# Kernel optimization log

Hardware: AMD Instinct MI355X
Metric: run time of the kernel (lower is better)

## Reference

```python
import jax, jax.numpy as jnp
import numpy as np

IN_NC = 7


def setup_inputs() -> dict:
    key = jax.random.key(0)
    ks = jax.random.split(key, 32)
    B, H, W = 4, 192, 192
    Cf, O, L = 64, 64, 32  # in_fea, out_fea, len=max(64//16,32)
    d = {}
    d['fea'] = jax.random.normal(ks[0], (B, Cf, H, W), jnp.float32)
    d['inputs'] = jax.random.normal(ks[1], (B, IN_NC, H, W), jnp.float32)
    j = 2
    for i in range(3):
        k = 2 * i + 1
        oc = IN_NC * 3 * k * k
        d['dw_w%d' % i] = jax.random.normal(ks[j], (Cf, 1, k, k), jnp.float32) * 0.05; j += 1
        d['dw_b%d' % i] = jnp.zeros((Cf,), jnp.float32)
        d['pw_w%d' % i] = jax.random.normal(ks[j], (oc, Cf), jnp.float32) * 0.05; j += 1
        d['pw_b%d' % i] = jnp.zeros((oc,), jnp.float32)
        d['dcn_w%d' % i] = jax.random.normal(ks[j], (O, IN_NC, k, k), jnp.float32) * 0.05; j += 1
        d['dcn_b%d' % i] = jnp.zeros((O,), jnp.float32)
    d['attn_w'] = jax.random.normal(ks[j], (O, 3 * O), jnp.float32) * 0.05; j += 1
    d['attn_b'] = jnp.zeros((O,), jnp.float32)
    d['fc_w'] = jax.random.normal(ks[j], (L, O), jnp.float32) * 0.05; j += 1
    d['fc_b'] = jnp.zeros((L,), jnp.float32)
    for i in range(3):
        d['fcs_w%d' % i] = jax.random.normal(ks[j], (O, L), jnp.float32) * 0.05; j += 1
        d['fcs_b%d' % i] = jnp.zeros((O,), jnp.float32)
    d['conv_w'] = jax.random.normal(ks[j], (O, 3 * O), jnp.float32) * 0.05; j += 1
    d['conv_b'] = jnp.zeros((O,), jnp.float32)
    return d


def _dw_conv(x, w, b):
    # depthwise conv, stride 1, SAME padding (pad = k//2 for odd k)
    y = jax.lax.conv_general_dilated(x, w, window_strides=(1, 1), padding='SAME',
                                     dimension_numbers=('NCHW', 'OIHW', 'NCHW'),
                                     feature_group_count=x.shape[1])
    return y + b[None, :, None, None]


def _pw_conv(x, w, b):
    return jnp.einsum('bchw,oc->bohw', x, w) + b[None, :, None, None]


def _mdcn(x, offset, mask, w, b, k):
    # Modulated deformable conv, deformable_groups == C (one channel per group),
    # stride 1, padding k//2. offset: [B, C*2*K, H, W] as (c, k, (dy,dx)); mask: [B, C*K, H, W].
    B, C, H, W = x.shape
    K = k * k
    pad = k // 2
    off = offset.reshape(B, C, K, 2, H, W)
    m = mask.reshape(B, C, K, H, W)
    ky = (jnp.arange(K) // k).astype(jnp.float32)
    kx = (jnp.arange(K) % k).astype(jnp.float32)
    py = off[:, :, :, 0] + (ky[:, None, None] + jnp.arange(H, dtype=jnp.float32)[None, :, None] - pad)
    px = off[:, :, :, 1] + (kx[:, None, None] + jnp.arange(W, dtype=jnp.float32)[None, None, :] - pad)
    y0 = jnp.floor(py)
    x0 = jnp.floor(px)
    wy = py - y0
    wx = px - x0
    bi = jnp.arange(B)[:, None, None, None, None]
    ci = jnp.arange(C)[None, :, None, None, None]

    def gather(yi, xi):
        valid = (yi >= 0) & (yi < H) & (xi >= 0) & (xi < W)
        yc = jnp.clip(yi, 0, H - 1).astype(jnp.int32)
        xc = jnp.clip(xi, 0, W - 1).astype(jnp.int32)
        return jnp.where(valid, x[bi, ci, yc, xc], 0.0)

    v00 = gather(y0, x0)
    v01 = gather(y0, x0 + 1)
    v10 = gather(y0 + 1, x0)
    v11 = gather(y0 + 1, x0 + 1)
    samp = (v00 * (1 - wy) * (1 - wx) + v01 * (1 - wy) * wx
            + v10 * wy * (1 - wx) + v11 * wy * wx) * m  # [B,C,K,H,W]
    O = w.shape[0]
    return jnp.einsum('bckhw,ock->bohw', samp, w.reshape(O, C, K)) + b[None, :, None, None]


def reference(fea, inputs,
              dw_w0, dw_b0, pw_w0, pw_b0, dcn_w0, dcn_b0,
              dw_w1, dw_b1, pw_w1, pw_b1, dcn_w1, dcn_b1,
              dw_w2, dw_b2, pw_w2, pw_b2, dcn_w2, dcn_b2,
              attn_w, attn_b, fc_w, fc_b,
              fcs_w0, fcs_b0, fcs_w1, fcs_b1, fcs_w2, fcs_b2,
              conv_w, conv_b):
    dw_w = [dw_w0, dw_w1, dw_w2]; dw_b = [dw_b0, dw_b1, dw_b2]
    pw_w = [pw_w0, pw_w1, pw_w2]; pw_b = [pw_b0, pw_b1, pw_b2]
    dcn_w = [dcn_w0, dcn_w1, dcn_w2]; dcn_b = [dcn_b0, dcn_b1, dcn_b2]
    fcs_w = [fcs_w0, fcs_w1, fcs_w2]; fcs_b = [fcs_b0, fcs_b1, fcs_b2]
    outs = []
    for i in range(3):
        k = 2 * i + 1
        ds = k * k
        om = _pw_conv(_dw_conv(fea, dw_w[i], dw_b[i]), pw_w[i], pw_b[i])
        offset = om[:, :IN_NC * 2 * ds]
        mask = jax.nn.sigmoid(om[:, IN_NC * 2 * ds:])
        outs.append(jax.nn.relu(_mdcn(inputs, offset, mask, dcn_w[i], dcn_b[i], k)))
    out = jnp.stack(outs, axis=1)  # [B, 3, O, H, W]
    B, T, C, H, W = out.shape
    att = jax.nn.relu(_pw_conv(out.reshape(B, T * C, H, W), attn_w, attn_b))
    att = jnp.mean(att, axis=(2, 3), keepdims=True)  # GAP -> [B, O, 1, 1]
    att = jax.nn.relu(_pw_conv(att, fc_w, fc_b))      # [B, L, 1, 1]
    atts = jnp.stack([_pw_conv(att, fcs_w[i], fcs_b[i]) for i in range(3)], axis=1)  # [B,3,O,1,1]
    out = out * atts
    out = jax.nn.relu(_pw_conv(out.reshape(B, T * C, H, W), conv_w, conv_b))
    return out
```

## Files before the change

### kernel.cpp

```cpp
#include <hip/hip_runtime.h>
#include <math.h>

#define HH 192
#define WW 192
#define HWP (192*192)
#define BB 4
#define CF 64
#define NC 7
#define OO 64
#define NTOT (BB*HWP)
#define PIX_BLOCKS (HWP/256)
#define PBLK2 (HWP/128)

typedef float f32x16 __attribute__((ext_vector_type(16)));
typedef float f32x4  __attribute__((ext_vector_type(4)));

template<int k>
__global__ __launch_bounds__(256)
void dwv_kernel(const float* __restrict__ fea, const float* __restrict__ w,
                const float* __restrict__ bias, float* __restrict__ out) {
    constexpr int pad = k / 2;
    int idx = blockIdx.x * 256 + threadIdx.x;
    int xq = idx % 48;
    int x0 = xq * 4;
    int hpos = (idx / 48) % HH;
    int plane = idx / (48 * HH);
    int c = plane % CF;
    const float* f = fea + (size_t)plane * HWP;

    float wk[k * k];
#pragma unroll
    for (int i = 0; i < k * k; ++i) wk[i] = w[c * k * k + i];

    float acc0 = 0.f, acc1 = 0.f, acc2 = 0.f, acc3 = 0.f;
#pragma unroll
    for (int dy = 0; dy < k; ++dy) {
        int y = hpos + dy - pad;
        if (y < 0 || y >= HH) continue;
        const float* row = f + y * WW;
        float4 q0 = (x0 >= 4) ? *(const float4*)(row + x0 - 4) : make_float4(0.f, 0.f, 0.f, 0.f);
        float4 q1 = *(const float4*)(row + x0);
        float4 q2 = (x0 + 4 < WW) ? *(const float4*)(row + x0 + 4) : make_float4(0.f, 0.f, 0.f, 0.f);
        float wnd[8] = {q0.z, q0.w, q1.x, q1.y, q1.z, q1.w, q2.x, q2.y};
#pragma unroll
        for (int dx = 0; dx < k; ++dx) {
            float wt = wk[dy * k + dx];
            acc0 += wnd[0 + dx + 2 - pad] * wt;
            acc1 += wnd[1 + dx + 2 - pad] * wt;
            acc2 += wnd[2 + dx + 2 - pad] * wt;
            acc3 += wnd[3 + dx + 2 - pad] * wt;
        }
    }
    float b = bias[c];
    float4 o = make_float4(acc0 + b, acc1 + b, acc2 + b, acc3 + b);
    *(float4*)(out + (size_t)plane * HWP + hpos * WW + x0) = o;
}

__global__ void transpose_kernel(const float* __restrict__ in, float* __restrict__ out,
                                 int rows, int cols) {
    int idx = blockIdx.x * 256 + threadIdx.x;
    if (idx >= rows * cols) return;
    int r = idx / cols, c = idx % cols;
    out[c * rows + r] = in[idx];
}

__global__ void k1_fold_kernel(const float* __restrict__ pw_w, const float* __restrict__ pw_b,
                               const float* __restrict__ dw_w0, const float* __restrict__ dw_b0,
                               float* __restrict__ pw_wf, float* __restrict__ pw_bf) {
    int i = blockIdx.x * 256 + threadIdx.x;
    if (i < 21 * 64) pw_wf[i] = pw_w[i] * dw_w0[i & 63];
    if (i < 21) {
        float s = pw_b[i];
        for (int c = 0; c < 64; ++c) s += pw_w[i * 64 + c] * dw_b0[c];
        pw_bf[i] = s;
    }
}

__global__ __launch_bounds__(256)
void pw_gemm_kernel(const float* __restrict__ pw_w, const float* __restrict__ pw_b,
                    const float* __restrict__ dw, float* __restrict__ om,
                    int src0, int n_yx, int src1, int M) {
    __shared__ float As[64][68];
    __shared__ float Bs[64][132];
    const int ntiles = NTOT / 128;
    int ntile = blockIdx.x % ntiles;
    int mtile = blockIdx.x / ntiles;
    int nb0 = ntile * 128;
    int mb0 = mtile * 64;
    int tid = threadIdx.x;

    {
        int m = tid & 63;
        int kq = tid >> 6;
        int gm = mb0 + m;
        int srow = (gm < M) ? ((gm < n_yx) ? (src0 + gm) : (src1 + (gm - n_yx))) : src0;
        const float* ap = pw_w + (size_t)srow * CF;
#pragma unroll
        for (int i = 0; i < 4; ++i) {
            int k0 = (kq * 4 + i) * 4;
            float4 v = *(const float4*)(ap + k0);
            As[k0 + 0][m] = v.x; As[k0 + 1][m] = v.y;
            As[k0 + 2][m] = v.z; As[k0 + 3][m] = v.w;
        }
    }
    {
        int b = nb0 / HWP;
        int p0 = nb0 % HWP;
        const float* bp = dw + (size_t)b * CF * HWP + p0;
#pragma unroll
        for (int i = 0; i < 8; ++i) {
            int idx = tid + i * 256;
            int kk = idx >> 5;
            int f4 = idx & 31;
            float4 v = *(const float4*)(bp + (size_t)kk * HWP + f4 * 4);
            *(float4*)&Bs[kk][f4 * 4] = v;
        }
    }
    __syncthreads();

    int tm = (tid & 15) * 4;
    int tn = (tid >> 4) * 8;
    f32x4 aA0 = 0.f, aA1 = 0.f, aB0 = 0.f, aB1 = 0.f;
    f32x4 aC0 = 0.f, aC1 = 0.f, aD0 = 0.f, aD1 = 0.f;
#pragma unroll 8
    for (int kk = 0; kk < 64; ++kk) {
        f32x4 a  = *(const f32x4*)&As[kk][tm];
        f32x4 b0 = *(const f32x4*)&Bs[kk][tn];
        f32x4 b1 = *(const f32x4*)&Bs[kk][tn + 4];
#pragma unroll
        for (int j = 0; j < 4; ++j) {
            aA0[j] += a[0] * b0[j];  aA1[j] += a[0] * b1[j];
            aB0[j] += a[1] * b0[j];  aB1[j] += a[1] * b1[j];
            aC0[j] += a[2] * b0[j];  aC1[j] += a[2] * b1[j];
            aD0[j] += a[3] * b0[j];  aD1[j] += a[3] * b1[j];
        }
    }
    {
        int gm = mb0 + tm;
        float* dst = om + (size_t)gm * NTOT + nb0 + tn;
        if (gm < M) {
            float bi = pw_b[(gm < n_yx) ? (src0 + gm) : (src1 + gm - n_yx)];
#pragma unroll
            for (int j = 0; j < 4; ++j) { dst[j] = aA0[j] + bi; dst[4 + j] = aA1[j] + bi; }
        }
        gm++; dst += NTOT;
        if (gm < M) {
            float bi = pw_b[(gm < n_yx) ? (src0 + gm) : (src1 + gm - n_yx)];
#pragma unroll
            for (int j = 0; j < 4; ++j) { dst[j] = aB0[j] + bi; dst[4 + j] = aB1[j] + bi; }
        }
        gm++; dst += NTOT;
        if (gm < M) {
            float bi = pw_b[(gm < n_yx) ? (src0 + gm) : (src1 + gm - n_yx)];
#pragma unroll
            for (int j = 0; j < 4; ++j) { dst[j] = aC0[j] + bi; dst[4 + j] = aC1[j] + bi; }
        }
        gm++; dst += NTOT;
        if (gm < M) {
            float bi = pw_b[(gm < n_yx) ? (src0 + gm) : (src1 + gm - n_yx)];
#pragma unroll
            for (int j = 0; j < 4; ++j) { dst[j] = aD0[j] + bi; dst[4 + j] = aD1[j] + bi; }
        }
    }
}

template<int k>
__global__ __launch_bounds__(256)
void sample_kernel(const float* __restrict__ om, const float* __restrict__ inputs,
                   float* __restrict__ sbuf, int t0, int t1) {
    constexpr int K = k * k;
    constexpr int pad = k / 2;
    const int T = t1 - t0;
    int g = blockIdx.x / (NTOT / 256);
    int nb = blockIdx.x % (NTOT / 256);
    int n = nb * 256 + threadIdx.x;
    int b = n / HWP, p = n % HWP;
    int h = p / WW, wq = p % WW;
    const float* inb = inputs + (size_t)b * NC * HWP;
    int half = (T + 1) >> 1;
    int i0 = g * half;
    int i1 = min(T, i0 + half);
#pragma unroll 2
    for (int i = i0; i < i1; ++i) {
        int r = t0 + i;
        float oy = om[(size_t)(2 * i) * NTOT + n];
        float ox = om[(size_t)(2 * i + 1) * NTOT + n];
        float mr = om[(size_t)(2 * T + i) * NTOT + n];
        int c = r / K;
        int kk = r - c * K;
        int ky = kk / k, kx = kk - ky * k;
        const float* inc_ = inb + (size_t)c * HWP;
        float m = 1.f / (1.f + __expf(-mr));
        float py = oy + (float)(ky + h - pad);
        float px = ox + (float)(kx + wq - pad);
        float y0 = floorf(py), x0 = floorf(px);
        float wyf = py - y0, wxf = px - x0;
        int iy0 = (int)y0, ix0 = (int)x0;
        bool y0v = (iy0 >= 0) && (iy0 < HH);
        bool y1v = (iy0 + 1 >= 0) && (iy0 + 1 < HH);
        bool x0v = (ix0 >= 0) && (ix0 < WW);
        bool x1v = (ix0 + 1 >= 0) && (ix0 + 1 < WW);
        int yc0 = min(max(iy0, 0), HH - 1), yc1 = min(max(iy0 + 1, 0), HH - 1);
        int xc0 = min(max(ix0, 0), WW - 1), xc1 = min(max(ix0 + 1, 0), WW - 1);
        float v00 = 0.f, v01 = 0.f, v10 = 0.f, v11 = 0.f;
        if (y0v) {
            if (x0v) v00 = inc_[yc0 * WW + xc0];
            if (x1v) v01 = inc_[yc0 * WW + xc1];
        }
        if (y1v) {
            if (x0v) v10 = inc_[yc1 * WW + xc0];
            if (x1v) v11 = inc_[yc1 * WW + xc1];
        }
        float s = (v00 * (1.f - wyf) * (1.f - wxf) + v01 * (1.f - wyf) * wxf +
                   v10 * wyf * (1.f - wxf) + v11 * wyf * wxf) * m;
        sbuf[(size_t)i * NTOT + n] = s;
    }
}

__global__ __launch_bounds__(256)
void acc_gemm_kernel(const float* __restrict__ wt,
                     const float* __restrict__ bias,
                     const float* __restrict__ sbuf,
                     float* __restrict__ outbuf, int t_slot,
                     int t0, int t1, int flags) {
    __shared__ float As[64][68];
    __shared__ float Bs[64][132];
    const int T = t1 - t0;
    int nb0 = blockIdx.x * 128;
    int tid = threadIdx.x;

    for (int i4 = tid; i4 < T * 16; i4 += 256) {
        int row = i4 >> 4, c4 = (i4 & 15) * 4;
        float4 v = *(const float4*)(wt + (size_t)(t0 + row) * OO + c4);
        As[row][c4] = v.x; As[row][c4 + 1] = v.y; As[row][c4 + 2] = v.z; As[row][c4 + 3] = v.w;
    }
    for (int i4 = tid; i4 < T * 32; i4 += 256) {
        int row = i4 >> 5, f4 = (i4 & 31) * 4;
        float4 v = *(const float4*)(sbuf + (size_t)row * NTOT + nb0 + f4);
        *(float4*)&Bs[row][f4] = v;
    }
    __syncthreads();

    int tm = (tid & 15) * 4;
    int tn = (tid >> 4) * 8;
    f32x4 aA0 = 0.f, aA1 = 0.f, aB0 = 0.f, aB1 = 0.f;
    f32x4 aC0 = 0.f, aC1 = 0.f, aD0 = 0.f, aD1 = 0.f;
#pragma unroll 2
    for (int kk = 0; kk < T; ++kk) {
        f32x4 a  = *(const f32x4*)&As[kk][tm];
        f32x4 b0 = *(const f32x4*)&Bs[kk][tn];
        f32x4 b1 = *(const f32x4*)&Bs[kk][tn + 4];
#pragma unroll
        for (int j = 0; j < 4; ++j) {
            aA0[j] += a[0] * b0[j];  aA1[j] += a[0] * b1[j];
            aB0[j] += a[1] * b0[j];  aB1[j] += a[1] * b1[j];
            aC0[j] += a[2] * b0[j];  aC1[j] += a[2] * b1[j];
            aD0[j] += a[3] * b0[j];  aD1[j] += a[3] * b1[j];
        }
    }

    int b = nb0 / HWP, p0 = nb0 % HWP;
    f32x4 accs[8] = {aA0, aA1, aB0, aB1, aC0, aC1, aD0, aD1};
#pragma unroll
    for (int row = 0; row < 4; ++row) {
        int ch = tm + row;
        float* ptr = outbuf + ((size_t)((b * 3 + t_slot) * OO + ch)) * HWP + p0 + tn;
        f32x4 lo = accs[row * 2], hi = accs[row * 2 + 1];
        if (!(flags & 1)) {
            f32x4 o0 = *(const f32x4*)ptr;
            f32x4 o1 = *(const f32x4*)(ptr + 4);
#pragma unroll
            for (int j = 0; j < 4; ++j) { lo[j] += o0[j]; hi[j] += o1[j]; }
        }
        if (flags & 2) {
            float bi = bias[ch];
#pragma unroll
            for (int j = 0; j < 4; ++j) {
                lo[j] += bi; hi[j] += bi;
                lo[j] = lo[j] > 0.f ? lo[j] : 0.f;
                hi[j] = hi[j] > 0.f ? hi[j] : 0.f;
            }
        }
        *(f32x4*)ptr = lo;
        *(f32x4*)(ptr + 4) = hi;
    }
}

__global__ __launch_bounds__(256)
void branch_k1_kernel(const float* __restrict__ fea,
                      const float* __restrict__ dw_w0, const float* __restrict__ dw_b0,
                      const float* __restrict__ pw_w, const float* __restrict__ pw_b,
                      const float* __restrict__ inputs,
                      const float* __restrict__ dcn_wt, const float* __restrict__ dcn_b,
                      float* __restrict__ outbuf) {
    __shared__ float lw[21 * 64];
    for (int i = threadIdx.x; i < 21 * 16; i += 256)
        ((float4*)lw)[i] = ((const float4*)pw_w)[i];
    __syncthreads();
    int gid = blockIdx.x;
    int b = gid / PIX_BLOCKS;
    int p = (gid % PIX_BLOCKS) * 256 + threadIdx.x;
    int h = p / WW, wq = p % WW;
    const float* inb = inputs + (size_t)b * NC * HWP;

    f32x16 dwv0, dwv1, dwv2, dwv3;
    {
        const float* fp = fea + (size_t)(b * CF) * HWP + p;
#pragma unroll
        for (int j = 0; j < 16; ++j) dwv0[j] = fp[(size_t)j * HWP] * dw_w0[j] + dw_b0[j];
#pragma unroll
        for (int j = 0; j < 16; ++j) dwv1[j] = fp[(size_t)(16 + j) * HWP] * dw_w0[16 + j] + dw_b0[16 + j];
#pragma unroll
        for (int j = 0; j < 16; ++j) dwv2[j] = fp[(size_t)(32 + j) * HWP] * dw_w0[32 + j] + dw_b0[32 + j];
#pragma unroll
        for (int j = 0; j < 16; ++j) dwv3[j] = fp[(size_t)(48 + j) * HWP] * dw_w0[48 + j] + dw_b0[48 + j];
    }
    f32x16 acc0, acc1, acc2, acc3;
#pragma unroll
    for (int j = 0; j < 16; ++j) { acc0[j] = 0.f; acc1[j] = 0.f; acc2[j] = 0.f; acc3[j] = 0.f; }

    for (int r = 0; r < NC; ++r) {
        const float* wy = lw + (2 * r) * 64;
        const float* wx = wy + 64;
        const float* wm = lw + (14 + r) * 64;
        const float* inc_ = inb + (size_t)r * HWP;
        float oy = pw_b[2 * r], ox = pw_b[2 * r + 1], om = pw_b[14 + r];
#pragma unroll
        for (int j = 0; j < 16; ++j) { oy += wy[j] * dwv0[j];      ox += wx[j] * dwv0[j];      om += wm[j] * dwv0[j]; }
#pragma unroll
        for (int j = 0; j < 16; ++j) { oy += wy[16 + j] * dwv1[j]; ox += wx[16 + j] * dwv1[j]; om += wm[16 + j] * dwv1[j]; }
#pragma unroll
        for (int j = 0; j < 16; ++j) { oy += wy[32 + j] * dwv2[j]; ox += wx[32 + j] * dwv2[j]; om += wm[32 + j] * dwv2[j]; }
#pragma unroll
        for (int j = 0; j < 16; ++j) { oy += wy[48 + j] * dwv3[j]; ox += wx[48 + j] * dwv3[j]; om += wm[48 + j] * dwv3[j]; }
        float m = 1.f / (1.f + __expf(-om));
        float py = oy + (float)h;
        float px = ox + (float)wq;
        float y0 = floorf(py), x0 = floorf(px);
        float wyf = py - y0, wxf = px - x0;
        int iy0 = (int)y0, ix0 = (int)x0;
        bool y0v = (iy0 >= 0) && (iy0 < HH);
        bool y1v = (iy0 + 1 >= 0) && (iy0 + 1 < HH);
        bool x0v = (ix0 >= 0) && (ix0 < WW);
        bool x1v = (ix0 + 1 >= 0) && (ix0 + 1 < WW);
        int yc0 = min(max(iy0, 0), HH - 1), yc1 = min(max(iy0 + 1, 0), HH - 1);
        int xc0 = min(max(ix0, 0), WW - 1), xc1 = min(max(ix0 + 1, 0), WW - 1);
        float v00 = 0.f, v01 = 0.f, v10 = 0.f, v11 = 0.f;
        if (y0v) {
            if (x0v) v00 = inc_[yc0 * WW + xc0];
            if (x1v) v01 = inc_[yc0 * WW + xc1];
        }
        if (y1v) {
            if (x0v) v10 = inc_[yc1 * WW + xc0];
            if (x1v) v11 = inc_[yc1 * WW + xc1];
        }
        float s = (v00 * (1.f - wyf) * (1.f - wxf) + v01 * (1.f - wyf) * wxf +
                   v10 * wyf * (1.f - wxf) + v11 * wyf * wxf) * m;
        const float* dt = dcn_wt + (size_t)r * OO;
#pragma unroll
        for (int j = 0; j < 16; ++j) acc0[j] += s * dt[j];
#pragma unroll
        for (int j = 0; j < 16; ++j) acc1[j] += s * dt[16 + j];
#pragma unroll
        for (int j = 0; j < 16; ++j) acc2[j] += s * dt[32 + j];
#pragma unroll
        for (int j = 0; j < 16; ++j) acc3[j] += s * dt[48 + j];
    }
    float* op = outbuf + (size_t)(b * 3 * OO) * HWP + p;
#pragma unroll
    for (int j = 0; j < 16; ++j) { float v = acc0[j] + dcn_b[j];      op[(size_t)j * HWP] = v > 0.f ? v : 0.f; }
#pragma unroll
    for (int j = 0; j < 16; ++j) { float v = acc1[j] + dcn_b[16 + j]; op[(size_t)(16 + j) * HWP] = v > 0.f ? v : 0.f; }
#pragma unroll
    for (int j = 0; j < 16; ++j) { float v = acc2[j] + dcn_b[32 + j]; op[(size_t)(32 + j) * HWP] = v > 0.f ? v : 0.f; }
#pragma unroll
    for (int j = 0; j < 16; ++j) { float v = acc3[j] + dcn_b[48 + j]; op[(size_t)(48 + j) * HWP] = v > 0.f ? v : 0.f; }
}

__global__ __launch_bounds__(256)
void attn_gemm_kernel(const float* __restrict__ outbuf, const float* __restrict__ attn_wt,
                      const float* __restrict__ attn_b, float* __restrict__ partial) {
    __shared__ float As[32][68];
    __shared__ float Bs[32][132];
    __shared__ float red[16][68];
    int nb0 = blockIdx.x * 128;
    int b = nb0 / HWP, p0 = nb0 % HWP;
    int tid = threadIdx.x;
    int tm = (tid & 15) * 4;
    int tn = (tid >> 4) * 8;

    f32x4 aA0 = 0.f, aA1 = 0.f, aB0 = 0.f, aB1 = 0.f;
    f32x4 aC0 = 0.f, aC1 = 0.f, aD0 = 0.f, aD1 = 0.f;
    for (int kc = 0; kc < 6; ++kc) {
        for (int i4 = tid; i4 < 32 * 16; i4 += 256) {
            int row = i4 >> 4, c4 = (i4 & 15) * 4;
            float4 v = *(const float4*)(attn_wt + (size_t)(kc * 32 + row) * OO + c4);
            As[row][c4] = v.x; As[row][c4 + 1] = v.y; As[row][c4 + 2] = v.z; As[row][c4 + 3] = v.w;
        }
        const float* bp = outbuf + ((size_t)(b * 192 + kc * 32)) * HWP + p0;
        for (int i4 = tid; i4 < 32 * 32; i4 += 256) {
            int row = i4 >> 5, f4 = (i4 & 31) * 4;
            float4 v = *(const float4*)(bp + (size_t)row * HWP + f4);
            *(float4*)&Bs[row][f4] = v;
        }
        __syncthreads();
#pragma unroll 4
        for (int kk = 0; kk < 32; ++kk) {
            f32x4 a  = *(const f32x4*)&As[kk][tm];
            f32x4 b0 = *(const f32x4*)&Bs[kk][tn];
            f32x4 b1 = *(const f32x4*)&Bs[kk][tn + 4];
#pragma unroll
            for (int j = 0; j < 4; ++j) {
                aA0[j] += a[0] * b0[j];  aA1[j] += a[0] * b1[j];
                aB0[j] += a[1] * b0[j];  aB1[j] += a[1] * b1[j];
                aC0[j] += a[2] * b0[j];  aC1[j] += a[2] * b1[j];
                aD0[j] += a[3] * b0[j];  aD1[j] += a[3] * b1[j];
            }
        }
        __syncthreads();
    }
    float bsum[4];
    {
        f32x4 accs[8] = {aA0, aA1, aB0, aB1, aC0, aC1, aD0, aD1};
#pragma unroll
        for (int row = 0; row < 4; ++row) {
            float bi = attn_b[tm + row];
            float s = 0.f;
#pragma unroll
            for (int j = 0; j < 4; ++j) {
                float v0 = accs[row * 2][j] + bi;
                float v1 = accs[row * 2 + 1][j] + bi;
                s += (v0 > 0.f ? v0 : 0.f) + (v1 > 0.f ? v1 : 0.f);
            }
            bsum[row] = s;
        }
    }
    int pg = tid >> 4;
#pragma unroll
    for (int row = 0; row < 4; ++row) red[pg][tm + row] = bsum[row];
    __syncthreads();
    if (tid < 64) {
        float s = 0.f;
#pragma unroll
        for (int g = 0; g < 16; ++g) s += red[g][tid];
        int lb = p0 / 128;
        partial[((size_t)(b * PBLK2 + lb)) * OO + tid] = s;
    }
}

__global__ void attn_finish_kernel(const float* __restrict__ partial,
                                   const float* __restrict__ fc_w, const float* __restrict__ fc_b,
                                   const float* __restrict__ fcs_w0, const float* __restrict__ fcs_b0,
                                   const float* __restrict__ fcs_w1, const float* __restrict__ fcs_b1,
                                   const float* __restrict__ fcs_w2, const float* __restrict__ fcs_b2,
                                   float* __restrict__ atts) {
    int b = blockIdx.x;
    __shared__ float attm[OO];
    __shared__ float fcv[32];
    int tid = threadIdx.x;
    if (tid < OO) {
        float s = 0.f;
        for (int blk = 0; blk < PBLK2; ++blk)
            s += partial[((size_t)(b * PBLK2 + blk)) * OO + tid];
        attm[tid] = s / (float)HWP;
    }
    __syncthreads();
    if (tid < 32) {
        float s = fc_b[tid];
        for (int o = 0; o < OO; ++o) s += fc_w[tid * OO + o] * attm[o];
        fcv[tid] = s > 0.f ? s : 0.f;
    }
    __syncthreads();
    if (tid < OO) {
        {
            float s = fcs_b0[tid];
            for (int j = 0; j < 32; ++j) s += fcs_w0[tid * 32 + j] * fcv[j];
            atts[b * 192 + 0 * OO + tid] = s;
        }
        {
            float s = fcs_b1[tid];
            for (int j = 0; j < 32; ++j) s += fcs_w1[tid * 32 + j] * fcv[j];
            atts[b * 192 + 1 * OO + tid] = s;
        }
        {
            float s = fcs_b2[tid];
            for (int j = 0; j < 32; ++j) s += fcs_w2[tid * 32 + j] * fcv[j];
            atts[b * 192 + 2 * OO + tid] = s;
        }
    }
}

__global__ __launch_bounds__(256)
void final_gemm_kernel(const float* __restrict__ outbuf, const float* __restrict__ atts,
                       const float* __restrict__ conv_wt, const float* __restrict__ conv_b,
                       float* __restrict__ out) {
    __shared__ float As[32][68];
    __shared__ float Bs[32][132];
    int nb0 = blockIdx.x * 128;
    int b = nb0 / HWP, p0 = nb0 % HWP;
    int tid = threadIdx.x;
    int tm = (tid & 15) * 4;
    int tn = (tid >> 4) * 8;
    const float* at = atts + b * 192;

    f32x4 aA0 = 0.f, aA1 = 0.f, aB0 = 0.f, aB1 = 0.f;
    f32x4 aC0 = 0.f, aC1 = 0.f, aD0 = 0.f, aD1 = 0.f;
    for (int kc = 0; kc < 6; ++kc) {
        for (int i4 = tid; i4 < 32 * 16; i4 += 256) {
            int row = i4 >> 4, c4 = (i4 & 15) * 4;
            float4 v = *(const float4*)(conv_wt + (size_t)(kc * 32 + row) * OO + c4);
            As[row][c4] = v.x; As[row][c4 + 1] = v.y; As[row][c4 + 2] = v.z; As[row][c4 + 3] = v.w;
        }
        const float* bp = outbuf + ((size_t)(b * 192 + kc * 32)) * HWP + p0;
        for (int i4 = tid; i4 < 32 * 32; i4 += 256) {
            int row = i4 >> 5, f4 = (i4 & 31) * 4;
            float sc = at[kc * 32 + row];
            float4 v = *(const float4*)(bp + (size_t)row * HWP + f4);
            Bs[row][f4] = v.x * sc; Bs[row][f4 + 1] = v.y * sc;
            Bs[row][f4 + 2] = v.z * sc; Bs[row][f4 + 3] = v.w * sc;
        }
        __syncthreads();
#pragma unroll 4
        for (int kk = 0; kk < 32; ++kk) {
            f32x4 a  = *(const f32x4*)&As[kk][tm];
            f32x4 b0 = *(const f32x4*)&Bs[kk][tn];
            f32x4 b1 = *(const f32x4*)&Bs[kk][tn + 4];
#pragma unroll
            for (int j = 0; j < 4; ++j) {
                aA0[j] += a[0] * b0[j];  aA1[j] += a[0] * b1[j];
                aB0[j] += a[1] * b0[j];  aB1[j] += a[1] * b1[j];
                aC0[j] += a[2] * b0[j];  aC1[j] += a[2] * b1[j];
                aD0[j] += a[3] * b0[j];  aD1[j] += a[3] * b1[j];
            }
        }
        __syncthreads();
    }
    f32x4 accs[8] = {aA0, aA1, aB0, aB1, aC0, aC1, aD0, aD1};
#pragma unroll
    for (int row = 0; row < 4; ++row) {
        int ch = tm + row;
        float bi = conv_b[ch];
        float* ptr = out + ((size_t)(b * OO + ch)) * HWP + p0 + tn;
        f32x4 lo = accs[row * 2], hi = accs[row * 2 + 1];
#pragma unroll
        for (int j = 0; j < 4; ++j) {
            lo[j] += bi; hi[j] += bi;
            lo[j] = lo[j] > 0.f ? lo[j] : 0.f;
            hi[j] = hi[j] > 0.f ? hi[j] : 0.f;
        }
        *(f32x4*)ptr = lo;
        *(f32x4*)(ptr + 4) = hi;
    }
}

extern "C" void kernel_launch(void* const* d_in, const int* in_sizes, int n_in,
                              void* d_out, int out_size, void* d_ws, size_t ws_size,
                              hipStream_t stream) {
    const float* fea    = (const float*)d_in[0];
    const float* inputs = (const float*)d_in[1];
    const float* dw_w[3]  = {(const float*)d_in[2],  (const float*)d_in[8],  (const float*)d_in[14]};
    const float* dw_b[3]  = {(const float*)d_in[3],  (const float*)d_in[9],  (const float*)d_in[15]};
    const float* pw_w[3]  = {(const float*)d_in[4],  (const float*)d_in[10], (const float*)d_in[16]};
    const float* pw_b[3]  = {(const float*)d_in[5],  (const float*)d_in[11], (const float*)d_in[17]};
    const float* dcn_w[3] = {(const float*)d_in[6],  (const float*)d_in[12], (const float*)d_in[18]};
    const float* dcn_b[3] = {(const float*)d_in[7],  (const float*)d_in[13], (const float*)d_in[19]};
    const float* attn_w = (const float*)d_in[20];
    const float* attn_b = (const float*)d_in[21];
    const float* fc_w   = (const float*)d_in[22];
    const float* fc_b   = (const float*)d_in[23];
    const float* fcs_w[3] = {(const float*)d_in[24], (const float*)d_in[26], (const float*)d_in[28]};
    const float* fcs_b[3] = {(const float*)d_in[25], (const float*)d_in[27], (const float*)d_in[29]};
    const float* conv_w = (const float*)d_in[30];
    const float* conv_b = (const float*)d_in[31];
    float* out = (float*)d_out;

    const size_t F_OUTBUF = (size_t)BB * 3 * OO * HWP;
    const size_t F_SMALL  = 73728 + 768 + 512 + 4096 + 11264 + 12288 + 12288 + 1344 + 32;
    float* W = (float*)d_ws;
    float* outbuf = W;            W += F_OUTBUF;
    size_t avail = (ws_size / 4 > F_OUTBUF + F_SMALL) ? (ws_size / 4 - F_OUTBUF - F_SMALL) : 0;
    int T = (int)(avail / (4 * (size_t)NTOT));
    if (T > 64) T = 64;
    if (T < 1) T = 1;
    float* om = W;                W += (size_t)3 * T * NTOT;
    float* sbuf = W;              W += (size_t)T * NTOT;
    float* partial = W;           W += 73728;
    float* atts = W;              W += 768;
    float* dcn_wt0 = W;           W += 512;
    float* dcn_wt1 = W;           W += 4096;
    float* dcn_wt2 = W;           W += 11264;
    float* attn_wt = W;           W += 12288;
    float* conv_wt = W;           W += 12288;
    float* pw_wf = W;             W += 1344;
    float* pw_bf = W;             W += 32;
    float* dwscr = out;

    transpose_kernel<<<(192 * 64 + 255) / 256, 256, 0, stream>>>(attn_w, attn_wt, 64, 192);
    transpose_kernel<<<(192 * 64 + 255) / 256, 256, 0, stream>>>(conv_w, conv_wt, 64, 192);
    transpose_kernel<<<(7 * 64 + 255) / 256, 256, 0, stream>>>(dcn_w[0], dcn_wt0, 64, 7);
    transpose_kernel<<<(63 * 64 + 255) / 256, 256, 0, stream>>>(dcn_w[1], dcn_wt1, 64, 63);
    transpose_kernel<<<(175 * 64 + 255) / 256, 256, 0, stream>>>(dcn_w[2], dcn_wt2, 64, 175);
    k1_fold_kernel<<<(21 * 64 + 255) / 256, 256, 0, stream>>>(pw_w[0], pw_b[0],
                                                              dw_w[0], dw_b[0], pw_wf, pw_bf);

    const int dwv_grid = (BB * CF * HH * 48) / 256;
    const int pix_grid = BB * PIX_BLOCKS;
    const int samp_grid = 2 * (NTOT / 256);
    const int acc_grid = NTOT / 128;
    const int ntiles = NTOT / 128;

    dwv_kernel<5><<<dwv_grid, 256, 0, stream>>>(fea, dw_w[2], dw_b[2], dwscr);
    {
        const int TT = 175;
        for (int t0 = 0; t0 < TT; t0 += T) {
            int t1 = (t0 + T < TT) ? (t0 + T) : TT;
            int Tc = t1 - t0, M = 3 * Tc;
            int mt = (M + 63) / 64;
            pw_gemm_kernel<<<mt * ntiles, 256, 0, stream>>>(pw_w[2], pw_b[2], dwscr, om,
                                                            2 * t0, 2 * Tc, 2 * TT + t0, M);
            sample_kernel<5><<<samp_grid, 256, 0, stream>>>(om, inputs, sbuf, t0, t1);
            int flags = (t0 == 0 ? 1 : 0) | (t1 == TT ? 2 : 0);
            acc_gemm_kernel<<<acc_grid, 256, 0, stream>>>(dcn_wt2, dcn_b[2], sbuf, outbuf,
                                                          2, t0, t1, flags);
        }
    }
    dwv_kernel<3><<<dwv_grid, 256, 0, stream>>>(fea, dw_w[1], dw_b[1], dwscr);
    {
        const int TT = 63;
        for (int t0 = 0; t0 < TT; t0 += T) {
            int t1 = (t0 + T < TT) ? (t0 + T) : TT;
            int Tc = t1 - t0, M = 3 * Tc;
            int mt = (M + 63) / 64;
            pw_gemm_kernel<<<mt * ntiles, 256, 0, stream>>>(pw_w[1], pw_b[1], dwscr, om,
                                                            2 * t0, 2 * Tc, 2 * TT + t0, M);
            sample_kernel<3><<<samp_grid, 256, 0, stream>>>(om, inputs, sbuf, t0, t1);
            int flags = (t0 == 0 ? 1 : 0) | (t1 == TT ? 2 : 0);
            acc_gemm_kernel<<<acc_grid, 256, 0, stream>>>(dcn_wt1, dcn_b[1], sbuf, outbuf,
                                                          1, t0, t1, flags);
        }
    }
    if (T >= 7) {
        pw_gemm_kernel<<<1 * ntiles, 256, 0, stream>>>(pw_wf, pw_bf, fea, om,
                                                       0, 14, 14, 21);
        sample_kernel<1><<<samp_grid, 256, 0, stream>>>(om, inputs, sbuf, 0, 7);
        acc_gemm_kernel<<<acc_grid, 256, 0, stream>>>(dcn_wt0, dcn_b[0], sbuf, outbuf,
                                                      0, 0, 7, 3);
    } else {
        branch_k1_kernel<<<pix_grid, 256, 0, stream>>>(fea, dw_w[0], dw_b[0], pw_w[0], pw_b[0],
                                                       inputs, dcn_wt0, dcn_b[0], outbuf);
    }

    attn_gemm_kernel<<<NTOT / 128, 256, 0, stream>>>(outbuf, attn_wt, attn_b, partial);
    attn_finish_kernel<<<BB, 64, 0, stream>>>(partial, fc_w, fc_b,
                                              fcs_w[0], fcs_b[0], fcs_w[1], fcs_b[1],
                                              fcs_w[2], fcs_b[2], atts);
    final_gemm_kernel<<<NTOT / 128, 256, 0, stream>>>(outbuf, atts, conv_wt, conv_b, out);
}
```

Before: 730.5 us.

## Fuse pointwise offset GEMM with bilinear sampling via shared memory

Merges the offset/mask pointwise GEMM and the deformable bilinear sampling into one kernel. Each 128-pixel tile computes 21 taps' offsets and masks (63 rows) into LDS, then samples directly, so the large om buffer is never written to or read back from global memory. The freed workspace lets the sample buffer hold more taps per accumulation GEMM, giving fewer acc_gemm launches. In exchange each 64-row GEMM tile fills only 63 rows, the dw activations are reread once per 21-tap group, and the branch_k1 fallback path is removed.

Measured after the change: 753.2 us. 1.03x slower.

```diff
diff --git a/kernel.cpp b/kernel.cpp
--- a/kernel.cpp
+++ b/kernel.cpp
@@ -9,11 +9,9 @@
 #define NC 7
 #define OO 64
 #define NTOT (BB*HWP)
-#define PIX_BLOCKS (HWP/256)
 #define PBLK2 (HWP/128)
 
-typedef float f32x16 __attribute__((ext_vector_type(16)));
-typedef float f32x4  __attribute__((ext_vector_type(4)));
+typedef float f32x4 __attribute__((ext_vector_type(4)));
 
 template<int k>
 __global__ __launch_bounds__(256)
@@ -76,28 +74,32 @@
     }
 }
 
+template<int k>
 __global__ __launch_bounds__(256)
-void pw_gemm_kernel(const float* __restrict__ pw_w, const float* __restrict__ pw_b,
-                    const float* __restrict__ dw, float* __restrict__ om,
-                    int src0, int n_yx, int src1, int M) {
+void pw_sample_kernel(const float* __restrict__ pw_w, const float* __restrict__ pw_b,
+                      const float* __restrict__ dw, const float* __restrict__ inputs,
+                      float* __restrict__ sbuf, int tap0, int ntap, int sb_row0, int TT) {
+    constexpr int K = k * k;
+    constexpr int pad = k / 2;
     __shared__ float As[64][68];
     __shared__ float Bs[64][132];
-    const int ntiles = NTOT / 128;
-    int ntile = blockIdx.x % ntiles;
-    int mtile = blockIdx.x / ntiles;
-    int nb0 = ntile * 128;
-    int mb0 = mtile * 64;
+    int nb0 = blockIdx.x * 128;
     int tid = threadIdx.x;
+    const int M = 3 * ntap;
 
     {
         int m = tid & 63;
         int kq = tid >> 6;
-        int gm = mb0 + m;
-        int srow = (gm < M) ? ((gm < n_yx) ? (src0 + gm) : (src1 + (gm - n_yx))) : src0;
+        int srow = 0;
+        if (m < M) {
+            int i = m / 3, q = m - 3 * i;
+            int r = tap0 + i;
+            srow = (q == 2) ? (2 * TT + r) : (2 * r + q);
+        }
         const float* ap = pw_w + (size_t)srow * CF;
 #pragma unroll
-        for (int i = 0; i < 4; ++i) {
-            int k0 = (kq * 4 + i) * 4;
+        for (int i2 = 0; i2 < 4; ++i2) {
+            int k0 = (kq * 4 + i2) * 4;
             float4 v = *(const float4*)(ap + k0);
             As[k0 + 0][m] = v.x; As[k0 + 1][m] = v.y;
             As[k0 + 2][m] = v.z; As[k0 + 3][m] = v.w;
@@ -108,8 +110,8 @@
         int p0 = nb0 % HWP;
         const float* bp = dw + (size_t)b * CF * HWP + p0;
 #pragma unroll
-        for (int i = 0; i < 8; ++i) {
-            int idx = tid + i * 256;
+        for (int i2 = 0; i2 < 8; ++i2) {
+            int idx = tid + i2 * 256;
             int kk = idx >> 5;
             int f4 = idx & 31;
             float4 v = *(const float4*)(bp + (size_t)kk * HWP + f4 * 4);
@@ -135,85 +137,69 @@
             aD0[j] += a[3] * b0[j];  aD1[j] += a[3] * b1[j];
         }
     }
-    {
-        int gm = mb0 + tm;
-        float* dst = om + (size_t)gm * NTOT + nb0 + tn;
-        if (gm < M) {
-            float bi = pw_b[(gm < n_yx) ? (src0 + gm) : (src1 + gm - n_yx)];
-#pragma unroll
-            for (int j = 0; j < 4; ++j) { dst[j] = aA0[j] + bi; dst[4 + j] = aA1[j] + bi; }
-        }
-        gm++; dst += NTOT;
-        if (gm < M) {
-            float bi = pw_b[(gm < n_yx) ? (src0 + gm) : (src1 + gm - n_yx)];
-#pragma unroll
-            for (int j = 0; j < 4; ++j) { dst[j] = aB0[j] + bi; dst[4 + j] = aB1[j] + bi; }
-        }
-        gm++; dst += NTOT;
-        if (gm < M) {
-            float bi = pw_b[(gm < n_yx) ? (src0 + gm) : (src1 + gm - n_yx)];
-#pragma unroll
-            for (int j = 0; j < 4; ++j) { dst[j] = aC0[j] + bi; dst[4 + j] = aC1[j] + bi; }
-        }
-        gm++; dst += NTOT;
-        if (gm < M) {
-            float bi = pw_b[(gm < n_yx) ? (src0 + gm) : (src1 + gm - n_yx)];
-#pragma unroll
-            for (int j = 0; j < 4; ++j) { dst[j] = aD0[j] + bi; dst[4 + j] = aD1[j] + bi; }
-        }
-    }
-}
-
-template<int k>
-__global__ __launch_bounds__(256)
-void sample_kernel(const float* __restrict__ om, const float* __restrict__ inputs,
-                   float* __restrict__ sbuf, int t0, int t1) {
-    constexpr int K = k * k;
-    constexpr int pad = k / 2;
-    const int T = t1 - t0;
-    int g = blockIdx.x / (NTOT / 256);
-    int nb = blockIdx.x % (NTOT / 256);
-    int n = nb * 256 + threadIdx.x;
-    int b = n / HWP, p = n % HWP;
-    int h = p / WW, wq = p % WW;
-    const float* inb = inputs + (size_t)b * NC * HWP;
-    int half = (T + 1) >> 1;
-    int i0 = g * half;
-    int i1 = min(T, i0 + half);
-#pragma unroll 2
-    for (int i = i0; i < i1; ++i) {
-        int r = t0 + i;
-        float oy = om[(size_t)(2 * i) * NTOT + n];
-        float ox = om[(size_t)(2 * i + 1) * NTOT + n];
-        float mr = om[(size_t)(2 * T + i) * NTOT + n];
-        int c = r / K;
-        int kk = r - c * K;
-        int ky = kk / k, kx = kk - ky * k;
-        const float* inc_ = inb + (size_t)c * HWP;
-        float m = 1.f / (1.f + __expf(-mr));
-        float py = oy + (float)(ky + h - pad);
-        float px = ox + (float)(kx + wq - pad);
-        float y0 = floorf(py), x0 = floorf(px);
-        float wyf = py - y0, wxf = px - x0;
-        int iy0 = (int)y0, ix0 = (int)x0;
-        bool y0v = (iy0 >= 0) && (iy0 < HH);
-        bool y1v = (iy0 + 1 >= 0) && (iy0 + 1 < HH);
-        bool x0v = (ix0 >= 0) && (ix0 < WW);
-        bool x1v = (ix0 + 1 >= 0) && (ix0 + 1 < WW);
-        int yc0 = min(max(iy0, 0), HH - 1), yc1 = min(max(iy0 + 1, 0), HH - 1);
-        int xc0 = min(max(ix0, 0), WW - 1), xc1 = min(max(ix0 + 1, 0), WW - 1);
-        float v00 = 0.f, v01 = 0.f, v10 = 0.f, v11 = 0.f;
-        if (y0v) {
-            if (x0v) v00 = inc_[yc0 * WW + xc0];
-            if (x1v) v01 = inc_[yc0 * WW + xc1];
-        }
-        if (y1v) {
-            if (x0v) v10 = inc_[yc1 * WW + xc0];
-            if (x1v) v11 = inc_[yc1 * WW + xc1];
-        }
-        float s = (v00 * (1.f - wyf) * (1.f - wxf) + v01 * (1.f - wyf) * wxf +
-                   v10 * wyf * (1.f - wxf) + v11 * wyf * wxf) * m;
-        sbuf[(size_t)i * NTOT + n] = s;
+    __syncthreads();
+
+    {
+        f32x4 accs[8] = {aA0, aA1, aB0, aB1, aC0, aC1, aD0, aD1};
+#pragma unroll
+        for (int row = 0; row < 4; ++row) {
+            int m = tm + row;
+            if (m < M) {
+                int i = m / 3, q = m - 3 * i;
+                int r = tap0 + i;
+                float bi = pw_b[(q == 2) ? (2 * TT + r) : (2 * r + q)];
+#pragma unroll
+                for (int j = 0; j < 4; ++j) {
+                    Bs[m][tn + j] = accs[row * 2][j] + bi;
+                    Bs[m][tn + 4 + j] = accs[row * 2 + 1][j] + bi;
+                }
+            }
+        }
+    }
+    __syncthreads();
+
+    {
+        int b = nb0 / HWP;
+        int p0 = nb0 % HWP;
+        int j = tid & 127;
+        int i0 = tid >> 7;
+        int p = p0 + j;
+        int h = p / WW, wq = p % WW;
+        const float* inb = inputs + (size_t)b * NC * HWP;
+        for (int i = i0; i < ntap; i += 2) {
+            int r = tap0 + i;
+            float oy = Bs[3 * i][j];
+            float ox = Bs[3 * i + 1][j];
+            float mr = Bs[3 * i + 2][j];
+            int c = r / K;
+            int kk = r - c * K;
+            int ky = kk / k, kx = kk - ky * k;
+            const float* inc_ = inb + (size_t)c * HWP;
+            float m = 1.f / (1.f + __expf(-mr));
+            float py = oy + (float)(ky + h - pad);
+            float px = ox + (float)(kx + wq - pad);
+            float y0 = floorf(py), x0 = floorf(px);
+            float wyf = py - y0, wxf = px - x0;
+            int iy0 = (int)y0, ix0 = (int)x0;
+            bool y0v = (iy0 >= 0) && (iy0 < HH);
+            bool y1v = (iy0 + 1 >= 0) && (iy0 + 1 < HH);
+            bool x0v = (ix0 >= 0) && (ix0 < WW);
+            bool x1v = (ix0 + 1 >= 0) && (ix0 + 1 < WW);
+            int yc0 = min(max(iy0, 0), HH - 1), yc1 = min(max(iy0 + 1, 0), HH - 1);
+            int xc0 = min(max(ix0, 0), WW - 1), xc1 = min(max(ix0 + 1, 0), WW - 1);
+            float v00 = 0.f, v01 = 0.f, v10 = 0.f, v11 = 0.f;
+            if (y0v) {
+                if (x0v) v00 = inc_[yc0 * WW + xc0];
+                if (x1v) v01 = inc_[yc0 * WW + xc1];
+            }
+            if (y1v) {
+                if (x0v) v10 = inc_[yc1 * WW + xc0];
+                if (x1v) v11 = inc_[yc1 * WW + xc1];
+            }
+            float s = (v00 * (1.f - wyf) * (1.f - wxf) + v01 * (1.f - wyf) * wxf +
+                       v10 * wyf * (1.f - wxf) + v11 * wyf * wxf) * m;
+            sbuf[(size_t)(sb_row0 + i) * NTOT + nb0 + j] = s;
+        }
     }
 }
 
@@ -284,97 +270,6 @@
         *(f32x4*)ptr = lo;
         *(f32x4*)(ptr + 4) = hi;
     }
-}
-
-__global__ __launch_bounds__(256)
-void branch_k1_kernel(const float* __restrict__ fea,
-                      const float* __restrict__ dw_w0, const float* __restrict__ dw_b0,
-                      const float* __restrict__ pw_w, const float* __restrict__ pw_b,
-                      const float* __restrict__ inputs,
-                      const float* __restrict__ dcn_wt, const float* __restrict__ dcn_b,
-                      float* __restrict__ outbuf) {
-    __shared__ float lw[21 * 64];
-    for (int i = threadIdx.x; i < 21 * 16; i += 256)
-        ((float4*)lw)[i] = ((const float4*)pw_w)[i];
-    __syncthreads();
-    int gid = blockIdx.x;
-    int b = gid / PIX_BLOCKS;
-    int p = (gid % PIX_BLOCKS) * 256 + threadIdx.x;
-    int h = p / WW, wq = p % WW;
-    const float* inb = inputs + (size_t)b * NC * HWP;
-
-    f32x16 dwv0, dwv1, dwv2, dwv3;
-    {
-        const float* fp = fea + (size_t)(b * CF) * HWP + p;
-#pragma unroll
-        for (int j = 0; j < 16; ++j) dwv0[j] = fp[(size_t)j * HWP] * dw_w0[j] + dw_b0[j];
-#pragma unroll
-        for (int j = 0; j < 16; ++j) dwv1[j] = fp[(size_t)(16 + j) * HWP] * dw_w0[16 + j] + dw_b0[16 + j];
-#pragma unroll
-        for (int j = 0; j < 16; ++j) dwv2[j] = fp[(size_t)(32 + j) * HWP] * dw_w0[32 + j] + dw_b0[32 + j];
-#pragma unroll
-        for (int j = 0; j < 16; ++j) dwv3[j] = fp[(size_t)(48 + j) * HWP] * dw_w0[48 + j] + dw_b0[48 + j];
-    }
-    f32x16 acc0, acc1, acc2, acc3;
-#pragma unroll
-    for (int j = 0; j < 16; ++j) { acc0[j] = 0.f; acc1[j] = 0.f; acc2[j] = 0.f; acc3[j] = 0.f; }
-
-    for (int r = 0; r < NC; ++r) {
-        const float* wy = lw + (2 * r) * 64;
-        const float* wx = wy + 64;
-        const float* wm = lw + (14 + r) * 64;
-        const float* inc_ = inb + (size_t)r * HWP;
-        float oy = pw_b[2 * r], ox = pw_b[2 * r + 1], om = pw_b[14 + r];
-#pragma unroll
-        for (int j = 0; j < 16; ++j) { oy += wy[j] * dwv0[j];      ox += wx[j] * dwv0[j];      om += wm[j] * dwv0[j]; }
-#pragma unroll
-        for (int j = 0; j < 16; ++j) { oy += wy[16 + j] * dwv1[j]; ox += wx[16 + j] * dwv1[j]; om += wm[16 + j] * dwv1[j]; }
-#pragma unroll
-        for (int j = 0; j < 16; ++j) { oy += wy[32 + j] * dwv2[j]; ox += wx[32 + j] * dwv2[j]; om += wm[32 + j] * dwv2[j]; }
-#pragma unroll
-        for (int j = 0; j < 16; ++j) { oy += wy[48 + j] * dwv3[j]; ox += wx[48 + j] * dwv3[j]; om += wm[48 + j] * dwv3[j]; }
-        float m = 1.f / (1.f + __expf(-om));
-        float py = oy + (float)h;
-        float px = ox + (float)wq;
-        float y0 = floorf(py), x0 = floorf(px);
-        float wyf = py - y0, wxf = px - x0;
-        int iy0 = (int)y0, ix0 = (int)x0;
-        bool y0v = (iy0 >= 0) && (iy0 < HH);
-        bool y1v = (iy0 + 1 >= 0) && (iy0 + 1 < HH);
-        bool x0v = (ix0 >= 0) && (ix0 < WW);
-        bool x1v = (ix0 + 1 >= 0) && (ix0 + 1 < WW);
-        int yc0 = min(max(iy0, 0), HH - 1), yc1 = min(max(iy0 + 1, 0), HH - 1);
-        int xc0 = min(max(ix0, 0), WW - 1), xc1 = min(max(ix0 + 1, 0), WW - 1);
-        float v00 = 0.f, v01 = 0.f, v10 = 0.f, v11 = 0.f;
-        if (y0v) {
-            if (x0v) v00 = inc_[yc0 * WW + xc0];
-            if (x1v) v01 = inc_[yc0 * WW + xc1];
-        }
-        if (y1v) {
-            if (x0v) v10 = inc_[yc1 * WW + xc0];
-            if (x1v) v11 = inc_[yc1 * WW + xc1];
-        }
-        float s = (v00 * (1.f - wyf) * (1.f - wxf) + v01 * (1.f - wyf) * wxf +
-                   v10 * wyf * (1.f - wxf) + v11 * wyf * wxf) * m;
-        const float* dt = dcn_wt + (size_t)r * OO;
-#pragma unroll
-        for (int j = 0; j < 16; ++j) acc0[j] += s * dt[j];
-#pragma unroll
-        for (int j = 0; j < 16; ++j) acc1[j] += s * dt[16 + j];
-#pragma unroll
-        for (int j = 0; j < 16; ++j) acc2[j] += s * dt[32 + j];
-#pragma unroll
-        for (int j = 0; j < 16; ++j) acc3[j] += s * dt[48 + j];
-    }
-    float* op = outbuf + (size_t)(b * 3 * OO) * HWP + p;
-#pragma unroll
-    for (int j = 0; j < 16; ++j) { float v = acc0[j] + dcn_b[j];      op[(size_t)j * HWP] = v > 0.f ? v : 0.f; }
-#pragma unroll
-    for (int j = 0; j < 16; ++j) { float v = acc1[j] + dcn_b[16 + j]; op[(size_t)(16 + j) * HWP] = v > 0.f ? v : 0.f; }
-#pragma unroll
-    for (int j = 0; j < 16; ++j) { float v = acc2[j] + dcn_b[32 + j]; op[(size_t)(32 + j) * HWP] = v > 0.f ? v : 0.f; }
-#pragma unroll
-    for (int j = 0; j < 16; ++j) { float v = acc3[j] + dcn_b[48 + j]; op[(size_t)(48 + j) * HWP] = v > 0.f ? v : 0.f; }
 }
 
 __global__ __launch_bounds__(256)
@@ -579,11 +474,10 @@
     float* W = (float*)d_ws;
     float* outbuf = W;            W += F_OUTBUF;
     size_t avail = (ws_size / 4 > F_OUTBUF + F_SMALL) ? (ws_size / 4 - F_OUTBUF - F_SMALL) : 0;
-    int T = (int)(avail / (4 * (size_t)NTOT));
-    if (T > 64) T = 64;
-    if (T < 1) T = 1;
-    float* om = W;                W += (size_t)3 * T * NTOT;
-    float* sbuf = W;              W += (size_t)T * NTOT;
+    int SB = (int)(avail / (size_t)NTOT);
+    if (SB > 63) SB = 63;
+    if (SB < 1) SB = 1;
+    float* sbuf = W;              W += (size_t)SB * NTOT;
     float* partial = W;           W += 73728;
     float* atts = W;              W += 768;
     float* dcn_wt0 = W;           W += 512;
@@ -604,50 +498,51 @@
                                                               dw_w[0], dw_b[0], pw_wf, pw_bf);
 
     const int dwv_grid = (BB * CF * HH * 48) / 256;
-    const int pix_grid = BB * PIX_BLOCKS;
-    const int samp_grid = 2 * (NTOT / 256);
-    const int acc_grid = NTOT / 128;
     const int ntiles = NTOT / 128;
 
     dwv_kernel<5><<<dwv_grid, 256, 0, stream>>>(fea, dw_w[2], dw_b[2], dwscr);
     {
         const int TT = 175;
-        for (int t0 = 0; t0 < TT; t0 += T) {
-            int t1 = (t0 + T < TT) ? (t0 + T) : TT;
-            int Tc = t1 - t0, M = 3 * Tc;
-            int mt = (M + 63) / 64;
-            pw_gemm_kernel<<<mt * ntiles, 256, 0, stream>>>(pw_w[2], pw_b[2], dwscr, om,
-                                                            2 * t0, 2 * Tc, 2 * TT + t0, M);
-            sample_kernel<5><<<samp_grid, 256, 0, stream>>>(om, inputs, sbuf, t0, t1);
-            int flags = (t0 == 0 ? 1 : 0) | (t1 == TT ? 2 : 0);
-            acc_gemm_kernel<<<acc_grid, 256, 0, stream>>>(dcn_wt2, dcn_b[2], sbuf, outbuf,
-                                                          2, t0, t1, flags);
+        for (int a0 = 0; a0 < TT; a0 += SB) {
+            int a1 = (a0 + SB < TT) ? (a0 + SB) : TT;
+            for (int tap0 = a0; tap0 < a1; tap0 += 21) {
+                int ntap = (tap0 + 21 < a1) ? 21 : (a1 - tap0);
+                pw_sample_kernel<5><<<ntiles, 256, 0, stream>>>(
+                    pw_w[2], pw_b[2], dwscr, inputs, sbuf, tap0, ntap, tap0 - a0, TT);
+            }
+            int flags = (a0 == 0 ? 1 : 0) | (a1 == TT ? 2 : 0);
+            acc_gemm_kernel<<<ntiles, 256, 0, stream>>>(dcn_wt2, dcn_b[2], sbuf, outbuf,
+                                                        2, a0, a1, flags);
         }
     }
     dwv_kernel<3><<<dwv_grid, 256, 0, stream>>>(fea, dw_w[1], dw_b[1], dwscr);
     {
         const int TT = 63;
-        for (int t0 = 0; t0 < TT; t0 += T) {
-            int t1 = (t0 + T < TT) ? (t0 + T) : TT;
-            int Tc = t1 - t0, M = 3 * Tc;
-            int mt = (M + 63) / 64;
-            pw_gemm_kernel<<<mt * ntiles, 256, 0, stream>>>(pw_w[1], pw_b[1], dwscr, om,
-                                                            2 * t0, 2 * Tc, 2 * TT + t0, M);
-            sample_kernel<3><<<samp_grid, 256, 0, stream>>>(om, inputs, sbuf, t0, t1);
-            int flags = (t0 == 0 ? 1 : 0) | (t1 == TT ? 2 : 0);
-            acc_gemm_kernel<<<acc_grid, 256, 0, stream>>>(dcn_wt1, dcn_b[1], sbuf, outbuf,
-                                                          1, t0, t1, flags);
-        }
-    }
-    if (T >= 7) {
-        pw_gemm_kernel<<<1 * ntiles, 256, 0, stream>>>(pw_wf, pw_bf, fea, om,
-                                                       0, 14, 14, 21);
-        sample_kernel<1><<<samp_grid, 256, 0, stream>>>(om, inputs, sbuf, 0, 7);
-        acc_gemm_kernel<<<acc_grid, 256, 0, stream>>>(dcn_wt0, dcn_b[0], sbuf, outbuf,
-                                                      0, 0, 7, 3);
-    } else {
-        branch_k1_kernel<<<pix_grid, 256, 0, stream>>>(fea, dw_w[0], dw_b[0], pw_w[0], pw_b[0],
-                                                       inputs, dcn_wt0, dcn_b[0], outbuf);
+        for (int a0 = 0; a0 < TT; a0 += SB) {
+            int a1 = (a0 + SB < TT) ? (a0 + SB) : TT;
+            for (int tap0 = a0; tap0 < a1; tap0 += 21) {
+                int ntap = (tap0 + 21 < a1) ? 21 : (a1 - tap0);
+                pw_sample_kernel<3><<<ntiles, 256, 0, stream>>>(
+                    pw_w[1], pw_b[1], dwscr, inputs, sbuf, tap0, ntap, tap0 - a0, TT);
+            }
+            int flags = (a0 == 0 ? 1 : 0) | (a1 == TT ? 2 : 0);
+            acc_gemm_kernel<<<ntiles, 256, 0, stream>>>(dcn_wt1, dcn_b[1], sbuf, outbuf,
+                                                        1, a0, a1, flags);
+        }
+    }
+    {
+        const int TT = 7;
+        for (int a0 = 0; a0 < TT; a0 += SB) {
+            int a1 = (a0 + SB < TT) ? (a0 + SB) : TT;
+            for (int tap0 = a0; tap0 < a1; tap0 += 21) {
+                int ntap = (tap0 + 21 < a1) ? 21 : (a1 - tap0);
+                pw_sample_kernel<1><<<ntiles, 256, 0, stream>>>(
+                    pw_wf, pw_bf, fea, inputs, sbuf, tap0, ntap, tap0 - a0, TT);
+            }
+            int flags = (a0 == 0 ? 1 : 0) | (a1 == TT ? 2 : 0);
+            acc_gemm_kernel<<<ntiles, 256, 0, stream>>>(dcn_wt0, dcn_b[0], sbuf, outbuf,
+                                                        0, a0, a1, flags);
+        }
     }
 
     attn_gemm_kernel<<<NTOT / 128, 256, 0, stream>>>(outbuf, attn_wt, attn_b, partial);
```
